# Kernel tuning notes

Hardware: AMD Instinct MI355X
Metric: run time of the kernel (lower is better)

## Reference

```python
import jax, jax.numpy as jnp
import numpy as np

D = 256
H = 8
HD = D // H
K = 10
CAP = 500000
B = 256


def setup_inputs() -> dict:
    key = jax.random.key(0)
    ks = jax.random.split(key, 5)
    return {
        "content": jax.random.normal(ks[0], (B, D), dtype=jnp.float32),
        "hologram": jax.random.normal(ks[1], (CAP, D), dtype=jnp.float32),
        "memory_strengths": jnp.ones((CAP,), dtype=jnp.float32),
        "in_proj_w": jax.random.normal(ks[2], (3 * D, D), dtype=jnp.float32) * (1.0 / np.sqrt(D)),
        "in_proj_b": jnp.zeros((3 * D,), dtype=jnp.float32),
        "out_proj_w": jax.random.normal(ks[3], (D, D), dtype=jnp.float32) * (1.0 / np.sqrt(D)),
        "out_proj_b": jnp.zeros((D,), dtype=jnp.float32),
    }


def reference(content, hologram, memory_strengths, in_proj_w, in_proj_b, out_proj_w, out_proj_b):
    # similarities [B, CAP], weighted by per-slot memory strength
    sims = jnp.matmul(content, hologram.T) * memory_strengths[None, :]
    # top-k memory slots per query
    top_vals, top_idx = jax.lax.top_k(sims, K)            # [B, K]
    mem = hologram[top_idx]                               # gather -> [B, K, D]

    # nn.MultiheadAttention (batch_first): packed in-proj split into q/k/v
    wq, wk, wv = in_proj_w[:D], in_proj_w[D:2 * D], in_proj_w[2 * D:]
    bq, bk, bv = in_proj_b[:D], in_proj_b[D:2 * D], in_proj_b[2 * D:]

    q = content @ wq.T + bq                               # [B, D]  (query len 1)
    k = mem @ wk.T + bk                                   # [B, K, D]
    v = mem @ wv.T + bv                                   # [B, K, D]

    qh = q.reshape(B, H, HD)                              # [B, H, HD]
    kh = k.reshape(B, K, H, HD).transpose(0, 2, 1, 3)     # [B, H, K, HD]
    vh = v.reshape(B, K, H, HD).transpose(0, 2, 1, 3)     # [B, H, K, HD]

    scores = jnp.einsum("bhd,bhkd->bhk", qh, kh) / np.sqrt(HD)
    attn = jax.nn.softmax(scores, axis=-1)                # [B, H, K]
    ctx = jnp.einsum("bhk,bhkd->bhd", attn, vh).reshape(B, D)
    recalled = ctx @ out_proj_w.T + out_proj_b            # [B, D]

    # torch MHA returns head-averaged attention weights; query len 1 squeezed
    attn_weights = attn.mean(axis=1)                      # [B, K]
    return recalled, attn_weights
```

## Files before the change

kernel.cpp:

```cpp
#include <hip/hip_runtime.h>
#include <hip/hip_bf16.h>
#include <math.h>

#define D      256
#define H      8
#define HD     32
#define TOPK   10
#define CAP    500000
#define BATCH  256

#define G1     256
#define T1     512
#define NT     32
#define ROUNDS 62
#define CHUNK  (NT*ROUNDS)
#define TOPB   16
#define MSEL   32

typedef float  f32x16 __attribute__((ext_vector_type(16)));
typedef __bf16 bf16x8 __attribute__((ext_vector_type(8)));

union FragCvt { uint4 u; bf16x8 v; };

__device__ __forceinline__ unsigned bfpair(float lo, float hi){
  unsigned a = __builtin_bit_cast(unsigned, lo);
  unsigned b = __builtin_bit_cast(unsigned, hi);
  a += 0x7FFFu + ((a >> 16) & 1u);
  b += 0x7FFFu + ((b >> 16) & 1u);
  return (a >> 16) | (b & 0xFFFF0000u);
}
__device__ __forceinline__ uint4 pack8(float4 p0, float4 p1){
  uint4 u;
  u.x = bfpair(p0.x, p0.y); u.y = bfpair(p0.z, p0.w);
  u.z = bfpair(p1.x, p1.y); u.w = bfpair(p1.z, p1.w);
  return u;
}

__device__ __forceinline__ void list_insert(float (&tv)[TOPB], int (&ti)[TOPB],
                                            float &minv, int &mins, float v, int gi){
  #pragma unroll
  for (int q = 0; q < TOPB; ++q){ if (q == mins){ tv[q] = v; ti[q] = gi; } }
  float mv = tv[0]; int ms = 0;
  #pragma unroll
  for (int q = 1; q < TOPB; ++q){
    float x = tv[q];
    if (x < mv){ mv = x; ms = q; }
  }
  minv = mv; mins = ms;
}

__device__ __forceinline__ void select16(const float* __restrict__ srow, int gbase, int lim,
                                         float (&tv)[TOPB], int (&ti)[TOPB],
                                         float &minv, int &mins){
  float sv[16];
  #pragma unroll
  for (int j = 0; j < 16; ++j) sv[j] = srow[j];
  unsigned pend = 0u;
  #pragma unroll
  for (int j = 0; j < 16; ++j) pend |= (sv[j] > minv) ? (1u << j) : 0u;
  unsigned limmask = (lim >= 16) ? 0xFFFFu : ((lim <= 0) ? 0u : ((1u << lim) - 1u));
  pend &= limmask;
  while (__any(pend != 0u)){
    if (pend){
      int j = __builtin_ctz(pend);
      pend &= pend - 1u;
      float v = -INFINITY;
      #pragma unroll
      for (int q = 0; q < 16; ++q) v = (q == j) ? sv[q] : v;
      if (v > minv) list_insert(tv, ti, minv, mins, v, gbase + j);
    }
  }
}

#define ROUND_BODY(R, PAR, I0,I1,I2,I3,IS, S0,S1,S2,S3,SS)                          \
  do {                                                                              \
    {                                              \
      int g  = n0 + ((R)+2)*NT + srow;                                              \
      int gc = (g < CAP) ? g : (CAP-1);                                             \
      int gb = gc*64 + scol*4;                                                      \
      I0 = hf4[gb+0]; I1 = hf4[gb+1]; I2 = hf4[gb+2]; I3 = hf4[gb+3];               \
      if (t < NT){                                                                  \
        int sidx = n0 + ((R)+2)*NT + t;                                             \
        IS = stren[(sidx < CAP) ? sidx : (CAP-1)];                                  \
      }                                                                             \
    }                                                                               \
    {                    \
      f32x16 acc = {0.f,0.f,0.f,0.f,0.f,0.f,0.f,0.f,                                \
                    0.f,0.f,0.f,0.f,0.f,0.f,0.f,0.f};                               \
      const int bbase = ml*32;                                                      \
      const int kxor  = ml & 7;                                                     \
      _Pragma("unroll")                                                             \
      for (int ks = 0; ks < 16; ++ks){                                              \
        FragCvt fb; fb.u = Bb[bufR][bbase + ((ks*2 + half) ^ kxor)];                \
        acc = __builtin_amdgcn_mfma_f32_32x32x16_bf16(afrag[ks], fb.v, acc, 0,0,0); \
      }                                                                             \
      float stren_ls = strenb[bufR][ml];                                            \
      _Pragma("unroll")                                                             \
      for (int reg = 0; reg < 16; ++reg){                                           \
        int rrow = (reg & 3) + 8*(reg >> 2) + 4*half;                               \
        simsb[PAR][(w*32 + rrow)*33 + ml] = acc[reg] * stren_ls;                    \
      }                                                                             \
    }                                                                               \
                           \
    if ((R) > 0){                                                                   \
      int nbp = n0 + ((R)-1)*NT;                                                    \
      select16(&simsb[(PAR)^1][row*33 + c0], nbp + c0, CAP - (nbp + c0),            \
               tv, ti, minv, mins);                                                 \
    }                                                                               \
    {                   \
      int kc0 = scol*2;                                                             \
      Bb[bufW][srow*32 + ((kc0  ) ^ (srow&7))] = pack8(S0, S1);                     \
      Bb[bufW][srow*32 + ((kc0+1) ^ (srow&7))] = pack8(S2, S3);                     \
      if (t < NT) strenb[bufW][t] = SS;                                             \
    }                                                                               \
    __syncthreads();                                                                \
    bufR = (bufR == 2) ? 0 : bufR + 1;                                              \
    bufW = (bufW == 2) ? 0 : bufW + 1;                                              \
  } while (0)

__global__ __launch_bounds__(T1) void k_score(
    const float* __restrict__ content, const float* __restrict__ holo,
    const float* __restrict__ stren, float* __restrict__ cand_val,
    int* __restrict__ cand_idx)
{
  __shared__ uint4 Bb[3][NT*32];
  __shared__ float simsb[2][BATCH*33];
  __shared__ float strenb[3][NT];

  const int t    = threadIdx.x;
  const int lane = t & 63;
  const int w    = t >> 6;
  const int half = lane >> 5;
  const int ml   = lane & 31;

  const int row = t & 255;
  const int c0  = (t >> 8) * 16;

  bf16x8 afrag[16];
  {
    const float4* cf4 = (const float4*)content;
    int base = (w*32 + ml)*64 + half*2;
    #pragma unroll
    for (int ks = 0; ks < 16; ++ks){
      float4 p0 = cf4[base + ks*4 + 0];
      float4 p1 = cf4[base + ks*4 + 1];
      FragCvt fc; fc.u = pack8(p0, p1);
      afrag[ks] = fc.v;
    }
  }

  float tv[TOPB]; int ti[TOPB];
  #pragma unroll
  for (int q = 0; q < TOPB; ++q){ tv[q] = -INFINITY; ti[q] = 0; }
  float minv = -INFINITY; int mins = 0;

  const int n0 = blockIdx.x * CHUNK;

  const int srow = t >> 4;
  const int scol = t & 15;
  const float4* hf4 = (const float4*)holo;

  float4 a0, a1, a2, a3, b0, b1, b2, b3;
  float  sa = 0.f, sb = 0.f;
  {
    int g  = n0 + srow;
    int gc = (g < CAP) ? g : (CAP-1);
    int gb = gc*64 + scol*4;
    a0 = hf4[gb+0]; a1 = hf4[gb+1]; a2 = hf4[gb+2]; a3 = hf4[gb+3];
    g  = n0 + NT + srow;
    gc = (g < CAP) ? g : (CAP-1);
    gb = gc*64 + scol*4;
    b0 = hf4[gb+0]; b1 = hf4[gb+1]; b2 = hf4[gb+2]; b3 = hf4[gb+3];
    if (t < NT){
      int s0 = n0 + t;
      sa = stren[(s0 < CAP) ? s0 : (CAP-1)];
      int s1 = n0 + NT + t;
      sb = stren[(s1 < CAP) ? s1 : (CAP-1)];
    }
    int kc0 = scol*2;
    Bb[0][srow*32 + ((kc0  ) ^ (srow&7))] = pack8(a0, a1);
    Bb[0][srow*32 + ((kc0+1) ^ (srow&7))] = pack8(a2, a3);
    if (t < NT) strenb[0][t] = sa;
  }
  __syncthreads();

  int bufR = 0, bufW = 1;
  for (int r = 0; r < ROUNDS; r += 2){
    ROUND_BODY(r,   0, a0,a1,a2,a3,sa,  b0,b1,b2,b3,sb);
    ROUND_BODY(r+1, 1, b0,b1,b2,b3,sb,  a0,a1,a2,a3,sa);
  }
  {
    const int lbuf = (ROUNDS-1) & 1;
    int nbl = n0 + (ROUNDS-1)*NT;
    select16(&simsb[lbuf][row*33 + c0], nbl + c0, CAP - (nbl + c0), tv, ti, minv, mins);
  }
  {
    float* mv_s = &simsb[0][0];
    int*   mi_s = (int*)&simsb[1][0];
    if (t >= 256){
      #pragma unroll
      for (int q = 0; q < TOPB; ++q){
        mv_s[row*33 + 16 + q] = tv[q];
        mi_s[row*33 + 16 + q] = ti[q];
      }
    }
    __syncthreads();
    if (t < 256){
      #pragma unroll
      for (int q = 0; q < TOPB; ++q){
        float v = mv_s[t*33 + 16 + q];
        int  gi = mi_s[t*33 + 16 + q];
        if (v > minv) list_insert(tv, ti, minv, mins, v, gi);
      }
      int base = t*(G1*TOPB) + blockIdx.x*TOPB;
      #pragma unroll
      for (int q = 0; q < TOPB; ++q){
        cand_val[base+q] = tv[q];
        cand_idx[base+q] = ti[q];
      }
    }
  }
}

__global__ void k_merge(const float* __restrict__ content,
                        const float* __restrict__ holo,
                        const float* __restrict__ stren,
                        const float* __restrict__ cand_val,
                        const int* __restrict__ cand_idx,
                        int* __restrict__ top_idx)
{
  const int row  = blockIdx.x;
  const int t    = threadIdx.x;
  const int lane = t & 63;
  const int w    = t >> 6;

  float cv[16]; int ci[16];
  {
    int base = row*(G1*TOPB);
    #pragma unroll
    for (int i = 0; i < 16; ++i){
      int c = i*256 + t;
      cv[i] = cand_val[base + c];
      ci[i] = cand_idx[base + c];
    }
  }
  __shared__ float  lv[4];
  __shared__ int    li[4];
  __shared__ int    sel[MSEL];
  __shared__ double ex[MSEL];
  __shared__ float  cont[D];

  for (int s = 0; s < MSEL; ++s){
    float bv = -INFINITY; int bi = 0x7FFFFFFF;
    #pragma unroll
    for (int i = 0; i < 16; ++i){
      if (cv[i] > bv || (cv[i] == bv && ci[i] < bi)){ bv = cv[i]; bi = ci[i]; }
    }
    #pragma unroll
    for (int off = 1; off < 64; off <<= 1){
      float ov = __shfl_xor(bv, off);
      int   oi = __shfl_xor(bi, off);
      if (ov > bv || (ov == bv && oi < bi)){ bv = ov; bi = oi; }
    }
    if (lane == 0){ lv[w] = bv; li[w] = bi; }
    __syncthreads();
    float wv = lv[0]; int wi = li[0];
    #pragma unroll
    for (int q = 1; q < 4; ++q){
      float ov = lv[q]; int oi = li[q];
      if (ov > wv || (ov == wv && oi < wi)){ wv = ov; wi = oi; }
    }
    if (t == 0) sel[s] = wi;
    #pragma unroll
    for (int i = 0; i < 16; ++i){ if (ci[i] == wi) cv[i] = -INFINITY; }
    __syncthreads();
  }
  if (t < 64) ((float4*)cont)[t] = ((const float4*)content)[row*64 + t];
  __syncthreads();

  const float4* hf4 = (const float4*)holo;
  float4 c4 = ((const float4*)cont)[lane];
  for (int q = 0; q < 8; ++q){
    int s   = w*8 + q;
    int idx = sel[s];
    float4 h4 = hf4[idx*64 + lane];
    double a = (double)h4.x*c4.x + (double)h4.y*c4.y + (double)h4.z*c4.z + (double)h4.w*c4.w;
    #pragma unroll
    for (int off = 1; off < 64; off <<= 1) a += __shfl_xor(a, off);
    if (lane == 0) ex[s] = a * (double)stren[idx];
  }
  __syncthreads();
  if (t == 0){
    unsigned used = 0;
    for (int r = 0; r < TOPK; ++r){
      int best = -1;
      for (int c = 0; c < MSEL; ++c){
        if (used & (1u << c)) continue;
        if (best < 0 || ex[c] > ex[best] || (ex[c] == ex[best] && sel[c] < sel[best])) best = c;
      }
      used |= (1u << best);
      top_idx[row*16 + r] = sel[best];
    }
  }
}

__global__ __launch_bounds__(512) void k_attn(
    const float* __restrict__ content, const float* __restrict__ holo,
    const float* __restrict__ inw, const float* __restrict__ inb,
    const float* __restrict__ outw, const float* __restrict__ outb,
    const int* __restrict__ top_idx, float* __restrict__ out)
{
  const int b = blockIdx.x;
  const int t = threadIdx.x;
  __shared__ float cont[D];
  __shared__ float mem_s[TOPK*D];
  __shared__ float q_s[D];
  __shared__ float k_s[TOPK*D];
  __shared__ float v_s[TOPK*D];
  __shared__ float sc[H*TOPK];
  __shared__ float at[H*TOPK];
  __shared__ float ctx[D];

  if (t < 64) ((float4*)cont)[t] = ((const float4*)content)[b*64 + t];
  for (int i = t; i < TOPK*D; i += 512){
    int j = i >> 8; int d = i & 255;
    mem_s[i] = holo[(size_t)top_idx[b*16 + j]*D + d];
  }
  __syncthreads();

  const float4* wf4 = (const float4*)inw;
  if (t < 256){
    float a = 0.f;
    const float4* c4p = (const float4*)cont;
    #pragma unroll 8
    for (int dc = 0; dc < 64; ++dc){
      float4 wv = wf4[t*64 + dc];
      float4 cc = c4p[dc];
      a += wv.x*cc.x + wv.y*cc.y + wv.z*cc.z + wv.w*cc.w;
    }
    q_s[t] = a + inb[t];
  }
  {
    int i    = (t < 256) ? t : (t - 256);
    int wrow = (t < 256) ? (256 + i) : (512 + i);
    float a[10];
    #pragma unroll
    for (int j = 0; j < 10; ++j) a[j] = 0.f;
    const float4* m4 = (const float4*)mem_s;
    for (int dc = 0; dc < 64; ++dc){
      float4 wv = wf4[wrow*64 + dc];
      #pragma unroll
      for (int j = 0; j < 10; ++j){
        float4 mm = m4[j*64 + dc];
        a[j] += wv.x*mm.x + wv.y*mm.y + wv.z*mm.z + wv.w*mm.w;
      }
    }
    float bias = inb[wrow];
    if (t < 256){
      #pragma unroll
      for (int j = 0; j < 10; ++j) k_s[j*256 + i] = a[j] + bias;
    } else {
      #pragma unroll
      for (int j = 0; j < 10; ++j) v_s[j*256 + i] = a[j] + bias;
    }
  }
  __syncthreads();
  if (t < H*TOPK){
    int h = t / TOPK, j = t % TOPK;
    float a = 0.f;
    #pragma unroll
    for (int d = 0; d < HD; ++d) a += q_s[h*HD + d] * k_s[j*256 + h*HD + d];
    sc[t] = a * 0.17677669529663687f;
  }
  __syncthreads();
  if (t < H){
    float m = -INFINITY;
    #pragma unroll
    for (int j = 0; j < 10; ++j) m = fmaxf(m, sc[t*10 + j]);
    float e[10]; float su = 0.f;
    #pragma unroll
    for (int j = 0; j < 10; ++j){ e[j] = expf(sc[t*10 + j] - m); su += e[j]; }
    float inv = 1.f / su;
    #pragma unroll
    for (int j = 0; j < 10; ++j) at[t*10 + j] = e[j]*inv;
  }
  __syncthreads();
  if (t < TOPK){
    float a = 0.f;
    #pragma unroll
    for (int h = 0; h < H; ++h) a += at[h*10 + t];
    out[BATCH*D + b*TOPK + t] = a * 0.125f;
  }
  if (t < 256){
    int h = t >> 5;
    float a = 0.f;
    #pragma unroll
    for (int j = 0; j < 10; ++j) a += at[h*10 + j] * v_s[j*256 + t];
    ctx[t] = a;
  }
  __syncthreads();
  if (t < 256){
    const float4* of4 = (const float4*)outw;
    const float4* c4p = (const float4*)ctx;
    float a = 0.f;
    #pragma unroll 8
    for (int dc = 0; dc < 64; ++dc){
      float4 wv = of4[t*64 + dc];
      float4 cc = c4p[dc];
      a += wv.x*cc.x + wv.y*cc.y + wv.z*cc.z + wv.w*cc.w;
    }
    out[b*D + t] = a + outb[t];
  }
}

extern "C" void kernel_launch(void* const* d_in, const int* in_sizes, int n_in,
                              void* d_out, int out_size, void* d_ws, size_t ws_size,
                              hipStream_t stream) {
  const float* content = (const float*)d_in[0];
  const float* holo    = (const float*)d_in[1];
  const float* stren   = (const float*)d_in[2];
  const float* inw     = (const float*)d_in[3];
  const float* inb     = (const float*)d_in[4];
  const float* outw    = (const float*)d_in[5];
  const float* outb    = (const float*)d_in[6];
  float* out = (float*)d_out;

  float* cand_val = (float*)d_ws;
  int*   cand_idx = (int*)(cand_val + BATCH*G1*TOPB);
  int*   top_idx  = (int*)(cand_idx + BATCH*G1*TOPB);

  hipLaunchKernelGGL(k_score, dim3(G1), dim3(T1), 0, stream,
                     content, holo, stren, cand_val, cand_idx);
  hipLaunchKernelGGL(k_merge, dim3(BATCH), dim3(256), 0, stream,
                     content, holo, stren, cand_val, cand_idx, top_idx);
  hipLaunchKernelGGL(k_attn, dim3(BATCH), dim3(512), 0, stream,
                     content, holo, inw, inb, outw, outb, top_idx, out);
}
```

Baseline: 919.4 us.

## Run top-k selection directly on MFMA accumulators instead of via shared memory

The MFMA operands are swapped so each lane's accumulator holds similarities for one query row against 16 hologram slots. Selection now runs straight from registers in the same round, which removes the shared-memory sims buffer, its write/read traffic and the one-round-delayed select. The two half-wave lists are merged with a lane shuffle at the end. Each lane keeps its own list for one query, and divergence in the insert loop stays. Freeing the large LDS buffer may also allow higher occupancy.

```diff
diff --git a/kernel.cpp b/kernel.cpp
--- a/kernel.cpp
+++ b/kernel.cpp
@@ -49,30 +49,7 @@
   minv = mv; mins = ms;
 }
 
-__device__ __forceinline__ void select16(const float* __restrict__ srow, int gbase, int lim,
-                                         float (&tv)[TOPB], int (&ti)[TOPB],
-                                         float &minv, int &mins){
-  float sv[16];
-  #pragma unroll
-  for (int j = 0; j < 16; ++j) sv[j] = srow[j];
-  unsigned pend = 0u;
-  #pragma unroll
-  for (int j = 0; j < 16; ++j) pend |= (sv[j] > minv) ? (1u << j) : 0u;
-  unsigned limmask = (lim >= 16) ? 0xFFFFu : ((lim <= 0) ? 0u : ((1u << lim) - 1u));
-  pend &= limmask;
-  while (__any(pend != 0u)){
-    if (pend){
-      int j = __builtin_ctz(pend);
-      pend &= pend - 1u;
-      float v = -INFINITY;
-      #pragma unroll
-      for (int q = 0; q < 16; ++q) v = (q == j) ? sv[q] : v;
-      if (v > minv) list_insert(tv, ti, minv, mins, v, gbase + j);
-    }
-  }
-}
-
-#define ROUND_BODY(R, PAR, I0,I1,I2,I3,IS, S0,S1,S2,S3,SS)                          \
+#define ROUND_BODY(R, I0,I1,I2,I3,IS, S0,S1,S2,S3,SS)                               \
   do {                                                                              \
     {                                              \
       int g  = n0 + ((R)+2)*NT + srow;                                              \
@@ -84,7 +61,7 @@
         IS = stren[(sidx < CAP) ? sidx : (CAP-1)];                                  \
       }                                                                             \
     }                                                                               \
-    {                    \
+    {         \
       f32x16 acc = {0.f,0.f,0.f,0.f,0.f,0.f,0.f,0.f,                                \
                     0.f,0.f,0.f,0.f,0.f,0.f,0.f,0.f};                               \
       const int bbase = ml*32;                                                      \
@@ -92,20 +69,42 @@
       _Pragma("unroll")                                                             \
       for (int ks = 0; ks < 16; ++ks){                                              \
         FragCvt fb; fb.u = Bb[bufR][bbase + ((ks*2 + half) ^ kxor)];                \
-        acc = __builtin_amdgcn_mfma_f32_32x32x16_bf16(afrag[ks], fb.v, acc, 0,0,0); \
+        acc = __builtin_amdgcn_mfma_f32_32x32x16_bf16(fb.v, afrag[ks], acc, 0,0,0); \
       }                                                                             \
-      float stren_ls = strenb[bufR][ml];                                            \
+      \
+      const float4* s4 = (const float4*)strenb[bufR];                               \
+      float4 sg0 = s4[0 + half], sg1 = s4[2 + half],                                \
+             sg2 = s4[4 + half], sg3 = s4[6 + half];                                \
+      float sv[16];                                                                 \
+      sv[ 0]=acc[ 0]*sg0.x; sv[ 1]=acc[ 1]*sg0.y; sv[ 2]=acc[ 2]*sg0.z;             \
+      sv[ 3]=acc[ 3]*sg0.w; sv[ 4]=acc[ 4]*sg1.x; sv[ 5]=acc[ 5]*sg1.y;             \
+      sv[ 6]=acc[ 6]*sg1.z; sv[ 7]=acc[ 7]*sg1.w; sv[ 8]=acc[ 8]*sg2.x;             \
+      sv[ 9]=acc[ 9]*sg2.y; sv[10]=acc[10]*sg2.z; sv[11]=acc[11]*sg2.w;             \
+      sv[12]=acc[12]*sg3.x; sv[13]=acc[13]*sg3.y; sv[14]=acc[14]*sg3.z;             \
+      sv[15]=acc[15]*sg3.w;                                                         \
+                 \
+      const int nbase = n0 + (R)*NT;                                                \
+      const bool full = (nbase + NT) <= CAP;                                        \
+      unsigned pend = 0u;                                                           \
       _Pragma("unroll")                                                             \
-      for (int reg = 0; reg < 16; ++reg){                                           \
-        int rrow = (reg & 3) + 8*(reg >> 2) + 4*half;                               \
-        simsb[PAR][(w*32 + rrow)*33 + ml] = acc[reg] * stren_ls;                    \
+      for (int j = 0; j < 16; ++j){                                                 \
+        int offj = (j & 3) + 8*(j >> 2) + 4*half;                                   \
+        bool ok = (sv[j] > minv) && (full || (nbase + offj) < CAP);                 \
+        pend |= ok ? (1u << j) : 0u;                                                \
       }                                                                             \
-    }                                                                               \
-                           \
-    if ((R) > 0){                                                                   \
-      int nbp = n0 + ((R)-1)*NT;                                                    \
-      select16(&simsb[(PAR)^1][row*33 + c0], nbp + c0, CAP - (nbp + c0),            \
-               tv, ti, minv, mins);                                                 \
+      while (__any(pend != 0u)){                                                    \
+        if (pend){                                                                  \
+          int j = __builtin_ctz(pend);                                              \
+          pend &= pend - 1u;                                                        \
+          float v = -INFINITY;                                                      \
+          _Pragma("unroll")                                                         \
+          for (int q = 0; q < 16; ++q) v = (q == j) ? sv[q] : v;                    \
+          if (v > minv){                                                            \
+            int gi = nbase + (j & 3) + 8*(j >> 2) + 4*half;                         \
+            list_insert(tv, ti, minv, mins, v, gi);                                 \
+          }                                                                         \
+        }                                                                           \
+      }                                                                             \
     }                                                                               \
     {                   \
       int kc0 = scol*2;                                                             \
@@ -124,7 +123,6 @@
     int* __restrict__ cand_idx)
 {
   __shared__ uint4 Bb[3][NT*32];
-  __shared__ float simsb[2][BATCH*33];
   __shared__ float strenb[3][NT];
 
   const int t    = threadIdx.x;
@@ -132,9 +130,6 @@
   const int w    = t >> 6;
   const int half = lane >> 5;
   const int ml   = lane & 31;
-
-  const int row = t & 255;
-  const int c0  = (t >> 8) * 16;
 
   bf16x8 afrag[16];
   {
@@ -186,38 +181,23 @@
 
   int bufR = 0, bufW = 1;
   for (int r = 0; r < ROUNDS; r += 2){
-    ROUND_BODY(r,   0, a0,a1,a2,a3,sa,  b0,b1,b2,b3,sb);
-    ROUND_BODY(r+1, 1, b0,b1,b2,b3,sb,  a0,a1,a2,a3,sa);
-  }
-  {
-    const int lbuf = (ROUNDS-1) & 1;
-    int nbl = n0 + (ROUNDS-1)*NT;
-    select16(&simsb[lbuf][row*33 + c0], nbl + c0, CAP - (nbl + c0), tv, ti, minv, mins);
-  }
-  {
-    float* mv_s = &simsb[0][0];
-    int*   mi_s = (int*)&simsb[1][0];
-    if (t >= 256){
-      #pragma unroll
-      for (int q = 0; q < TOPB; ++q){
-        mv_s[row*33 + 16 + q] = tv[q];
-        mi_s[row*33 + 16 + q] = ti[q];
-      }
-    }
-    __syncthreads();
-    if (t < 256){
-      #pragma unroll
-      for (int q = 0; q < TOPB; ++q){
-        float v = mv_s[t*33 + 16 + q];
-        int  gi = mi_s[t*33 + 16 + q];
-        if (v > minv) list_insert(tv, ti, minv, mins, v, gi);
-      }
-      int base = t*(G1*TOPB) + blockIdx.x*TOPB;
-      #pragma unroll
-      for (int q = 0; q < TOPB; ++q){
-        cand_val[base+q] = tv[q];
-        cand_idx[base+q] = ti[q];
-      }
+    ROUND_BODY(r,   a0,a1,a2,a3,sa,  b0,b1,b2,b3,sb);
+    ROUND_BODY(r+1, b0,b1,b2,b3,sb,  a0,a1,a2,a3,sa);
+  }
+
+  #pragma unroll
+  for (int q = 0; q < TOPB; ++q){
+    float ov = __shfl_xor(tv[q], 32);
+    int   oi = __shfl_xor(ti[q], 32);
+    if (half == 0 && ov > minv) list_insert(tv, ti, minv, mins, ov, oi);
+  }
+  if (half == 0){
+    int m    = w*32 + ml;
+    int base = m*(G1*TOPB) + blockIdx.x*TOPB;
+    #pragma unroll
+    for (int q = 0; q < TOPB; ++q){
+      cand_val[base+q] = tv[q];
+      cand_idx[base+q] = ti[q];
     }
   }
 }
```

Result: slower. 940.4 us (+2.3%).
